# Optimization experiments

Measured on AMD Instinct MI355X. Metric: run time of the kernel, lower is better.

## Reference

```python
import jax, jax.numpy as jnp
import numpy as np

NEG_SLOPE = 0.2
EPS = 1e-6


def setup_inputs() -> dict:
    key = jax.random.key(0)
    k1, k2 = jax.random.split(key)
    B, C, N = 4, 64, 32768
    x = jax.random.normal(k1, (B, C, 3, N), dtype=jnp.float32)
    # VNLinear weight: nn.Linear(in, out, bias=False).weight -> [out, in]
    W = jax.random.normal(k2, (C, C), dtype=jnp.float32) * (1.0 / np.sqrt(C))
    return {"x": x, "W": W}


def reference(x, W):
    # VNLinear: kron(W, eye(3)) conv2d == per-3-vector channel mix
    # d[b,o,v,n] = sum_i W[o,i] * x[b,i,v,n]
    d = jnp.einsum('oi,bivn->bovn', W, x)
    dotprod = jnp.sum(x * d, axis=2, keepdims=True)      # [B,C,1,N]
    d_norm_sq = jnp.sum(d * d, axis=2, keepdims=True)    # [B,C,1,N]
    neg = x - (1.0 - NEG_SLOPE) * (dotprod / (d_norm_sq + EPS)) * d
    return jnp.where(dotprod >= 0, x, neg)
```

## Files before the change

### kernel.cpp

```cpp
#include <hip/hip_runtime.h>

#define NEG_SLOPE 0.2f
#define EPS 1e-6f


#define C_CH 64
#define V_DIM 3
#define N_FULL 32768
#define NT 32
#define THREADS 256

typedef __attribute__((ext_vector_type(8))) short bf16x8;
typedef __attribute__((ext_vector_type(4))) float f32x4;

__device__ __forceinline__ ushort f2bf(float f) {
    union { float f; unsigned u; } v; v.f = f;
    unsigned r = v.u + 0x7FFFu + ((v.u >> 16) & 1u);
    return (ushort)(r >> 16);
}
__device__ __forceinline__ float bf2f(ushort s) {
    union { unsigned u; float f; } v; v.u = ((unsigned)s) << 16; return v.f;
}

__global__ void w_split_kernel(const float* __restrict__ W,
                               ushort* __restrict__ whi, ushort* __restrict__ wlo) {
    int i = blockIdx.x * 256 + threadIdx.x;
    if (i < C_CH * C_CH) {
        float w = W[i];
        ushort h = f2bf(w);
        whi[i] = h;
        wlo[i] = f2bf(w - bf2f(h));
    }
}

__device__ __forceinline__ int swz(int row) { return ((row >> 3) & 7) << 2; }

template<bool USE_WS>
__global__ __launch_bounds__(THREADS, 5)
void vn_mfma32(const float* __restrict__ x,
               const float* __restrict__ Wf,
               const ushort* __restrict__ whi, const ushort* __restrict__ wlo,
               float* __restrict__ out) {
    __shared__ unsigned xs[C_CH * V_DIM][NT];

    const int t    = threadIdx.x;
    const int tile = blockIdx.x;
    const int b    = tile >> 10;
    const int n0   = (tile & 1023) << 5;

    const float* xb = x + (size_t)b * (C_CH * V_DIM * N_FULL) + n0;

    const int lane = t & 63;
    const int w    = t >> 6;
    const int wo   = w >> 1;
    const int wn   = w & 1;
    const int l4   = lane & 15;
    const int hi   = lane >> 4;

    bf16x8 Ah[2][2], Al[2][2];
    if (USE_WS) {
        #pragma unroll
        for (int m = 0; m < 2; ++m)
            #pragma unroll
            for (int kh = 0; kh < 2; ++kh) {
                size_t off = (size_t)(wo * 32 + m * 16 + l4) * C_CH + kh * 32 + hi * 8;
                Ah[m][kh] = *(const bf16x8*)(whi + off);
                Al[m][kh] = *(const bf16x8*)(wlo + off);
            }
    } else {
        #pragma unroll
        for (int m = 0; m < 2; ++m)
            #pragma unroll
            for (int kh = 0; kh < 2; ++kh) {
                const float* wp = Wf + (size_t)(wo * 32 + m * 16 + l4) * C_CH + kh * 32 + hi * 8;
                float4 wa = *(const float4*)wp;
                float4 wb = *(const float4*)(wp + 4);
                float wf[8] = {wa.x, wa.y, wa.z, wa.w, wb.x, wb.y, wb.z, wb.w};
                bf16x8 h, l;
                #pragma unroll
                for (int j = 0; j < 8; ++j) {
                    ushort hb = f2bf(wf[j]);
                    h[j] = (short)hb;
                    l[j] = (short)f2bf(wf[j] - bf2f(hb));
                }
                Ah[m][kh] = h; Al[m][kh] = l;
            }
    }

    #pragma unroll
    for (int it = 0; it < 6; ++it) {
        int idx = t + it * THREADS;
        int row = idx >> 3;
        int c4  = (idx & 7) << 2;
        float4 v = *(const float4*)(xb + (size_t)row * N_FULL + c4);
        float vf[4] = {v.x, v.y, v.z, v.w};
        unsigned p[4];
        #pragma unroll
        for (int q = 0; q < 4; ++q) {
            ushort h = f2bf(vf[q]);
            ushort l = f2bf(vf[q] - bf2f(h));
            p[q] = ((unsigned)h << 16) | l;
        }
        *(uint4*)&xs[row][c4 ^ swz(row)] = *(const uint4*)p;
    }
    __syncthreads();

    f32x4 acc[2][3];
    #pragma unroll
    for (int m = 0; m < 2; ++m)
        #pragma unroll
        for (int v = 0; v < 3; ++v)
            acc[m][v] = (f32x4){0.f, 0.f, 0.f, 0.f};

    #pragma unroll
    for (int v = 0; v < 3; ++v) {
        #pragma unroll
        for (int kh = 0; kh < 2; ++kh) {
            bf16x8 bh, bl;
            #pragma unroll
            for (int j = 0; j < 8; ++j) {
                int row = (kh * 32 + hi * 8 + j) * V_DIM + v;
                unsigned p = xs[row][(wn * 16 + l4) ^ swz(row)];
                bh[j] = (short)(p >> 16);
                bl[j] = (short)(p & 0xffffu);
            }
            #pragma unroll
            for (int m = 0; m < 2; ++m) {
                acc[m][v] = __builtin_amdgcn_mfma_f32_16x16x32_bf16(Ah[m][kh], bh, acc[m][v], 0, 0, 0);
                acc[m][v] = __builtin_amdgcn_mfma_f32_16x16x32_bf16(Ah[m][kh], bl, acc[m][v], 0, 0, 0);
                acc[m][v] = __builtin_amdgcn_mfma_f32_16x16x32_bf16(Al[m][kh], bh, acc[m][v], 0, 0, 0);
            }
        }
    }

    const int n = wn * 16 + l4;
    float* ob = out + (size_t)b * (C_CH * V_DIM * N_FULL) + n0 + n;
    #pragma unroll
    for (int m = 0; m < 2; ++m) {
        #pragma unroll
        for (int r = 0; r < 4; ++r) {
            const int o = wo * 32 + m * 16 + hi * 4 + r;
            float xv[3], dv[3];
            #pragma unroll
            for (int v = 0; v < 3; ++v) {
                int row = o * V_DIM + v;
                unsigned p = xs[row][n ^ swz(row)];
                xv[v] = bf2f((ushort)(p >> 16)) + bf2f((ushort)(p & 0xffffu));
                dv[v] = acc[m][v][r];
            }
            float dot  = xv[0] * dv[0] + xv[1] * dv[1] + xv[2] * dv[2];
            float dnsq = dv[0] * dv[0] + dv[1] * dv[1] + dv[2] * dv[2];
            float f = (1.0f - NEG_SLOPE) * dot / (dnsq + EPS);
            float o0, o1, o2;
            if (dot >= 0.f) {
                o0 = xv[0]; o1 = xv[1]; o2 = xv[2];
            } else {
                o0 = xv[0] - f * dv[0]; o1 = xv[1] - f * dv[1]; o2 = xv[2] - f * dv[2];
            }
            float* op = ob + (size_t)o * (V_DIM * N_FULL);
            op[0 * N_FULL] = o0;
            op[1 * N_FULL] = o1;
            op[2 * N_FULL] = o2;
        }
    }
}

extern "C" void kernel_launch(void* const* d_in, const int* in_sizes, int n_in,
                              void* d_out, int out_size, void* d_ws, size_t ws_size,
                              hipStream_t stream) {
    const float* x = (const float*)d_in[0];
    const float* W = (const float*)d_in[1];
    float* out = (float*)d_out;

    const int B = 4;
    const int blocks = B * (N_FULL / NT);

    if (ws_size >= 2u * C_CH * C_CH * sizeof(ushort)) {
        ushort* whi = (ushort*)d_ws;
        ushort* wlo = whi + C_CH * C_CH;
        w_split_kernel<<<(C_CH * C_CH + 255) / 256, 256, 0, stream>>>(W, whi, wlo);
        vn_mfma32<true><<<blocks, THREADS, 0, stream>>>(x, W, whi, wlo, out);
    } else {
        vn_mfma32<false><<<blocks, THREADS, 0, stream>>>(x, W, nullptr, nullptr, out);
    }
}
```

Baseline: 46.35 us.

## Process four tiles per block with register prefetch of next tile

Result: slower. 72.73 us (+56.9%).

```diff
diff --git a/kernel.cpp b/kernel.cpp
--- a/kernel.cpp
+++ b/kernel.cpp
@@ -9,6 +9,7 @@
 #define N_FULL 32768
 #define NT 32
 #define THREADS 256
+#define TPB 4
 
 typedef __attribute__((ext_vector_type(8))) short bf16x8;
 typedef __attribute__((ext_vector_type(4))) float f32x4;
@@ -20,6 +21,16 @@
 }
 __device__ __forceinline__ float bf2f(ushort s) {
     union { unsigned u; float f; } v; v.u = ((unsigned)s) << 16; return v.f;
+}
+__device__ __forceinline__ unsigned pack_hl(float x) {
+    union { float f; unsigned u; } a; a.f = x;
+    unsigned uh = (a.u + 0x8000u) & 0xffff0000u;
+    union { unsigned u; float f; } hb; hb.u = uh;
+    union { float f; unsigned u; } rb; rb.f = x - hb.f;
+    return uh | (rb.u >> 16);
+}
+__device__ __forceinline__ float u2f(unsigned u) {
+    union { unsigned u; float f; } v; v.u = u; return v.f;
 }
 
 __global__ void w_split_kernel(const float* __restrict__ W,
@@ -36,7 +47,7 @@
 __device__ __forceinline__ int swz(int row) { return ((row >> 3) & 7) << 2; }
 
 template<bool USE_WS>
-__global__ __launch_bounds__(THREADS, 5)
+__global__ __launch_bounds__(THREADS, 4)
 void vn_mfma32(const float* __restrict__ x,
                const float* __restrict__ Wf,
                const ushort* __restrict__ whi, const ushort* __restrict__ wlo,
@@ -44,12 +55,6 @@
     __shared__ unsigned xs[C_CH * V_DIM][NT];
 
     const int t    = threadIdx.x;
-    const int tile = blockIdx.x;
-    const int b    = tile >> 10;
-    const int n0   = (tile & 1023) << 5;
-
-    const float* xb = x + (size_t)b * (C_CH * V_DIM * N_FULL) + n0;
-
     const int lane = t & 63;
     const int w    = t >> 6;
     const int wo   = w >> 1;
@@ -57,6 +62,9 @@
     const int l4   = lane & 15;
     const int hi   = lane >> 4;
 
+    const int srow = t >> 3;
+    const int sc4  = (t & 7) << 2;
+
     bf16x8 Ah[2][2], Al[2][2];
     if (USE_WS) {
         #pragma unroll
@@ -87,81 +95,99 @@
             }
     }
 
+    int tile = blockIdx.x * TPB;
+    const float* xb = x + (size_t)(tile >> 10) * (C_CH * V_DIM * N_FULL)
+                        + ((tile & 1023) << 5);
+    float4 pre[6];
     #pragma unroll
-    for (int it = 0; it < 6; ++it) {
-        int idx = t + it * THREADS;
-        int row = idx >> 3;
-        int c4  = (idx & 7) << 2;
-        float4 v = *(const float4*)(xb + (size_t)row * N_FULL + c4);
-        float vf[4] = {v.x, v.y, v.z, v.w};
-        unsigned p[4];
-        #pragma unroll
-        for (int q = 0; q < 4; ++q) {
-            ushort h = f2bf(vf[q]);
-            ushort l = f2bf(vf[q] - bf2f(h));
-            p[q] = ((unsigned)h << 16) | l;
-        }
-        *(uint4*)&xs[row][c4 ^ swz(row)] = *(const uint4*)p;
-    }
-    __syncthreads();
-
-    f32x4 acc[2][3];
+    for (int it = 0; it < 6; ++it)
+        pre[it] = *(const float4*)(xb + (size_t)(srow + it * 32) * N_FULL + sc4);
+
     #pragma unroll
-    for (int m = 0; m < 2; ++m)
-        #pragma unroll
-        for (int v = 0; v < 3; ++v)
-            acc[m][v] = (f32x4){0.f, 0.f, 0.f, 0.f};
-
-    #pragma unroll
-    for (int v = 0; v < 3; ++v) {
-        #pragma unroll
-        for (int kh = 0; kh < 2; ++kh) {
-            bf16x8 bh, bl;
-            #pragma unroll
-            for (int j = 0; j < 8; ++j) {
-                int row = (kh * 32 + hi * 8 + j) * V_DIM + v;
-                unsigned p = xs[row][(wn * 16 + l4) ^ swz(row)];
-                bh[j] = (short)(p >> 16);
-                bl[j] = (short)(p & 0xffffu);
-            }
-            #pragma unroll
-            for (int m = 0; m < 2; ++m) {
-                acc[m][v] = __builtin_amdgcn_mfma_f32_16x16x32_bf16(Ah[m][kh], bh, acc[m][v], 0, 0, 0);
-                acc[m][v] = __builtin_amdgcn_mfma_f32_16x16x32_bf16(Ah[m][kh], bl, acc[m][v], 0, 0, 0);
-                acc[m][v] = __builtin_amdgcn_mfma_f32_16x16x32_bf16(Al[m][kh], bh, acc[m][v], 0, 0, 0);
-            }
-        }
-    }
-
-    const int n = wn * 16 + l4;
-    float* ob = out + (size_t)b * (C_CH * V_DIM * N_FULL) + n0 + n;
-    #pragma unroll
-    for (int m = 0; m < 2; ++m) {
-        #pragma unroll
-        for (int r = 0; r < 4; ++r) {
-            const int o = wo * 32 + m * 16 + hi * 4 + r;
-            float xv[3], dv[3];
-            #pragma unroll
-            for (int v = 0; v < 3; ++v) {
-                int row = o * V_DIM + v;
-                unsigned p = xs[row][n ^ swz(row)];
-                xv[v] = bf2f((ushort)(p >> 16)) + bf2f((ushort)(p & 0xffffu));
-                dv[v] = acc[m][v][r];
-            }
-            float dot  = xv[0] * dv[0] + xv[1] * dv[1] + xv[2] * dv[2];
-            float dnsq = dv[0] * dv[0] + dv[1] * dv[1] + dv[2] * dv[2];
-            float f = (1.0f - NEG_SLOPE) * dot / (dnsq + EPS);
-            float o0, o1, o2;
-            if (dot >= 0.f) {
-                o0 = xv[0]; o1 = xv[1]; o2 = xv[2];
-            } else {
-                o0 = xv[0] - f * dv[0]; o1 = xv[1] - f * dv[1]; o2 = xv[2] - f * dv[2];
-            }
-            float* op = ob + (size_t)o * (V_DIM * N_FULL);
-            op[0 * N_FULL] = o0;
-            op[1 * N_FULL] = o1;
-            op[2 * N_FULL] = o2;
-        }
+    for (int tt = 0; tt < TPB; ++tt) {
+        if (tt) __syncthreads();
+
+        #pragma unroll
+        for (int it = 0; it < 6; ++it) {
+            int row = srow + it * 32;
+            float vf[4] = {pre[it].x, pre[it].y, pre[it].z, pre[it].w};
+            unsigned p[4];
+            #pragma unroll
+            for (int q = 0; q < 4; ++q) p[q] = pack_hl(vf[q]);
+            *(uint4*)&xs[row][sc4 ^ swz(row)] = *(const uint4*)p;
+        }
+
+        if (tt + 1 < TPB) {
+            int tn = tile + 1;
+            const float* xbn = x + (size_t)(tn >> 10) * (C_CH * V_DIM * N_FULL)
+                                 + ((tn & 1023) << 5);
+            #pragma unroll
+            for (int it = 0; it < 6; ++it)
+                pre[it] = *(const float4*)(xbn + (size_t)(srow + it * 32) * N_FULL + sc4);
+        }
+        __syncthreads();
+
+        f32x4 acc[2][3];
+        #pragma unroll
+        for (int m = 0; m < 2; ++m)
+            #pragma unroll
+            for (int v = 0; v < 3; ++v)
+                acc[m][v] = (f32x4){0.f, 0.f, 0.f, 0.f};
+
+        #pragma unroll
+        for (int v = 0; v < 3; ++v) {
+            #pragma unroll
+            for (int kh = 0; kh < 2; ++kh) {
+                bf16x8 bh, bl;
+                #pragma unroll
+                for (int j = 0; j < 8; ++j) {
+                    int row = (kh * 32 + hi * 8 + j) * V_DIM + v;
+                    unsigned p = xs[row][(wn * 16 + l4) ^ swz(row)];
+                    bh[j] = (short)(p >> 16);
+                    bl[j] = (short)(p & 0xffffu);
+                }
+                #pragma unroll
+                for (int m = 0; m < 2; ++m) {
+                    acc[m][v] = __builtin_amdgcn_mfma_f32_16x16x32_bf16(Ah[m][kh], bh, acc[m][v], 0, 0, 0);
+                    acc[m][v] = __builtin_amdgcn_mfma_f32_16x16x32_bf16(Ah[m][kh], bl, acc[m][v], 0, 0, 0);
+                    acc[m][v] = __builtin_amdgcn_mfma_f32_16x16x32_bf16(Al[m][kh], bh, acc[m][v], 0, 0, 0);
+                }
+            }
+        }
+
+        const int n = wn * 16 + l4;
+        float* ob = out + (size_t)(tile >> 10) * (C_CH * V_DIM * N_FULL)
+                        + ((tile & 1023) << 5) + n;
+        #pragma unroll
+        for (int m = 0; m < 2; ++m) {
+            #pragma unroll
+            for (int r = 0; r < 4; ++r) {
+                const int o = wo * 32 + m * 16 + hi * 4 + r;
+                float xv[3], dv[3];
+                #pragma unroll
+                for (int v = 0; v < 3; ++v) {
+                    int row = o * V_DIM + v;
+                    unsigned p = xs[row][n ^ swz(row)];
+                    xv[v] = u2f(p & 0xffff0000u) + u2f(p << 16);
+                    dv[v] = acc[m][v][r];
+                }
+                float dot  = xv[0] * dv[0] + xv[1] * dv[1] + xv[2] * dv[2];
+                float dnsq = dv[0] * dv[0] + dv[1] * dv[1] + dv[2] * dv[2];
+                float f = (1.0f - NEG_SLOPE) * dot / (dnsq + EPS);
+                float o0, o1, o2;
+                if (dot >= 0.f) {
+                    o0 = xv[0]; o1 = xv[1]; o2 = xv[2];
+                } else {
+                    o0 = xv[0] - f * dv[0]; o1 = xv[1] - f * dv[1]; o2 = xv[2] - f * dv[2];
+                }
+                float* op = ob + (size_t)o * (V_DIM * N_FULL);
+                op[0 * N_FULL] = o0;
+                op[1 * N_FULL] = o1;
+                op[2 * N_FULL] = o2;
+            }
+        }
+
+        ++tile;
     }
 }
 
@@ -173,7 +199,7 @@
     float* out = (float*)d_out;
 
     const int B = 4;
-    const int blocks = B * (N_FULL / NT);
+    const int blocks = B * (N_FULL / NT) / TPB;
 
     if (ws_size >= 2u * C_CH * C_CH * sizeof(ushort)) {
         ushort* whi = (ushort*)d_ws;
```
